# Kernel optimization log

Measured on AMD Instinct MI355X. Metric: run time of the kernel, lower is better.

The kernel has to match this reference:

```python
import jax, jax.numpy as jnp
import numpy as np

COST_CLASS, COST_MASK, COST_DICE = 2.0, 5.0, 5.0
NUM_POINTS = 12544

def setup_inputs() -> dict:
    key = jax.random.key(0)
    k1, k2, k3, k4, k5 = jax.random.split(key, 5)
    bs, Q, K = 4, 100, 134
    H = W = 256
    M = 80
    P = H * W
    pred_logits = jax.random.normal(k1, (bs, Q, K), dtype=jnp.float32)
    pred_masks = jax.random.normal(k2, (bs, Q, H, W), dtype=jnp.float32)
    tgt_labels = jax.random.randint(k3, (M,), 0, K - 1, dtype=jnp.int32)
    # binary target masks, stored as float (matches .float() in torch code)
    tgt_masks = (jax.random.uniform(k4, (M, H, W)) > 0.5).astype(jnp.float32)
    # random subset of points without replacement (torch.randperm[:num_points])
    point_idx = jax.random.permutation(k5, P)[:NUM_POINTS].astype(jnp.int32)
    return {"pred_logits": pred_logits, "pred_masks": pred_masks,
            "tgt_labels": tgt_labels, "tgt_masks": tgt_masks,
            "point_idx": point_idx}

def reference(pred_logits, pred_masks, tgt_labels, tgt_masks, point_idx):
    bs, Q, K = pred_logits.shape
    N = bs * Q
    M = tgt_masks.shape[0]
    Pn = point_idx.shape[0]

    # class cost: -p[n, tgt_id[m]]
    out_prob = jax.nn.softmax(pred_logits.reshape(N, K), axis=-1)
    tgt_ids = jnp.clip(tgt_labels.astype(jnp.int32), 0, K - 1)
    cost_class = -out_prob[:, tgt_ids]                      # (N, M)

    # sampled mask logits / targets
    x = pred_masks.reshape(N, -1)[:, point_idx]             # (N, Pn) logits
    y = tgt_masks.reshape(M, -1)[:, point_idx]              # (M, Pn) binary float

    # BCE-with-logits cost, separable form:
    # mean_p[softplus(x) - x*y] = mean_p softplus(x) - (x @ y^T)/Pn
    sp_mean = jnp.mean(jax.nn.softplus(x), axis=-1)         # (N,)
    xy = jnp.einsum('np,mp->nm', x, y)                      # (N, M)
    cost_mask = sp_mean[:, None] - xy / Pn

    # dice cost
    s = jax.nn.sigmoid(x)                                   # (N, Pn)
    numer = 2.0 * jnp.einsum('np,mp->nm', s, y)             # (N, M)
    denom = jnp.sum(s, axis=-1)[:, None] + jnp.sum(y, axis=-1)[None, :]
    cost_dice = 1.0 - (numer + 1.0) / (denom + 1.0)

    C = COST_CLASS * cost_class + COST_MASK * cost_mask + COST_DICE * cost_dice
    return C.reshape(bs, Q, M)
```

## Files before the change

kernel.cpp:

```cpp
#include <hip/hip_runtime.h>
#include <math.h>

#define N_ROWS 400
#define M_ROWS 80
#define K_CLS  134
#define PN     12544
#define PFULL  65536
#define NSUB   25
#define TSTEPS 392
#define KSPLIT 196
#define TPB    2

#define ZB_BLOCKS 33
#define GY_BLOCKS 245

typedef __attribute__((ext_vector_type(4))) float  f32x4;
typedef __attribute__((ext_vector_type(8))) __bf16 bf16x8;

__device__ __forceinline__ float wave_reduce_sum(float v) {
#pragma unroll
    for (int off = 32; off > 0; off >>= 1) v += __shfl_down(v, off, 64);
    return v;
}

__global__ __launch_bounds__(1024) void sort_softmax_kernel(
        const int* __restrict__ point_idx, int* __restrict__ sel,
        const float* __restrict__ pred_logits,
        float* __restrict__ rowmax, float* __restrict__ rowsum) {
    int tid = threadIdx.x;
    if (blockIdx.x == 0) {
        __shared__ unsigned int bits[PFULL / 32];
        __shared__ int wtot[16], wbase[16];
        bits[tid] = 0u; bits[tid + 1024] = 0u;
        __syncthreads();
        for (int i = tid; i < PN; i += 1024) {
            int p = point_idx[i];
            atomicOr(&bits[p >> 5], 1u << (p & 31));
        }
        __syncthreads();
        unsigned int w0 = bits[tid * 2], w1 = bits[tid * 2 + 1];
        int cnt = __popc(w0) + __popc(w1);
        int lane = tid & 63, wid = tid >> 6;
        int v = cnt;
#pragma unroll
        for (int off = 1; off < 64; off <<= 1) {
            int u = __shfl_up(v, off, 64);
            if (lane >= off) v += u;
        }
        if (lane == 63) wtot[wid] = v;
        __syncthreads();
        if (tid == 0) {
            int run = 0;
#pragma unroll
            for (int i = 0; i < 16; ++i) { wbase[i] = run; run += wtot[i]; }
        }
        __syncthreads();
        int base = wbase[wid] + (v - cnt);
        int p0 = tid * 64;
        while (w0) { int b = __builtin_ctz(w0); w0 &= w0 - 1; sel[base++] = p0 + b; }
        p0 += 32;
        while (w1) { int b = __builtin_ctz(w1); w1 &= w1 - 1; sel[base++] = p0 + b; }
    } else {
        int wave = tid >> 6, lane = tid & 63;
        int n = (blockIdx.x - 1) * 16 + wave;
        const float* row = pred_logits + n * K_CLS;
        float mx = -1e30f;
        for (int k = lane; k < K_CLS; k += 64) mx = fmaxf(mx, row[k]);
#pragma unroll
        for (int off = 32; off > 0; off >>= 1) mx = fmaxf(mx, __shfl_down(mx, off, 64));
        mx = __shfl(mx, 0, 64);
        float se = 0.f;
        for (int k = lane; k < K_CLS; k += 64) se += expf(row[k] - mx);
        se = wave_reduce_sum(se);
        if (lane == 0) { rowmax[n] = mx; rowsum[n] = se; }
    }
}

__global__ __launch_bounds__(512) void stage1b_kernel(
        const float* __restrict__ tgt_masks, const int* __restrict__ sel,
        __bf16* __restrict__ Yb, float* __restrict__ ypart,
        float* __restrict__ zero_region, int zero_n4) {
    __shared__ float smem[128];
    int b = blockIdx.x;
    if (b < ZB_BLOCKS) {
        int i = b * 512 + threadIdx.x;
        if (i < zero_n4) {
            f32x4 z = {0.f, 0.f, 0.f, 0.f};
            ((f32x4*)zero_region)[i] = z;
        }
        return;
    }
    int bb = b - ZB_BLOCKS;
    int j = bb / 49, tch = bb % 49;
    int wave = threadIdx.x >> 6, lane = threadIdx.x & 63;
    int colL = lane & 15, quad = lane >> 4;
    int m = 16 * j + colL;
    int t = tch * 8 + wave;
    int k0 = t * 32 + quad * 8;
    const float* yrow = tgt_masks + (size_t)m * PFULL;
    int idx[8];
    *(int4*)(idx)     = *(const int4*)(sel + k0);
    *(int4*)(idx + 4) = *(const int4*)(sel + k0 + 4);
    bf16x8 v; float acc = 0.f;
#pragma unroll
    for (int jj = 0; jj < 8; ++jj) {
        float y = yrow[idx[jj]];
        v[jj] = (__bf16)y;
        acc += y;
    }
    ((bf16x8*)Yb)[(size_t)(t * 5 + j) * 64 + lane] = v;
    acc += __shfl_down(acc, 32, 64);
    acc += __shfl_down(acc, 16, 64);
    if (quad == 0) smem[wave * 16 + colL] = acc;
    __syncthreads();
    if (threadIdx.x < 16) {
        float s = 0.f;
#pragma unroll
        for (int wv = 0; wv < 8; ++wv) s += smem[wv * 16 + threadIdx.x];
        ypart[tch * M_ROWS + 16 * j + threadIdx.x] = s;
    }
}

__global__ __launch_bounds__(256) void gemm_fused_kernel(
        const float* __restrict__ pred_masks, const int* __restrict__ sel,
        const __bf16* __restrict__ Yb,
        float* __restrict__ xyacc, float* __restrict__ syacc,
        float* __restrict__ spsum, float* __restrict__ ssum) {
    int wave = threadIdx.x >> 6, lane = threadIdx.x & 63;
    int flat = blockIdx.x * 4 + wave;
    int nsub = flat / KSPLIT, kc = flat % KSPLIT;
    int n0 = nsub * 16;
    int colL = lane & 15, quad = lane >> 4;
    int tbase = kc * TPB;

    const float* row = pred_masks + (size_t)(n0 + colL) * PFULL;
    const bf16x8* Yfrag = (const bf16x8*)Yb;

    f32x4 accX[5], accS[5];
    f32x4 zero = {0.f, 0.f, 0.f, 0.f};
#pragma unroll
    for (int j = 0; j < 5; ++j) { accX[j] = zero; accS[j] = zero; }
    float sumS = 0.f, sumSP = 0.f;

    float xs[TPB][8];
    bf16x8 Bbuf[TPB][5];
#pragma unroll
    for (int i = 0; i < TPB; ++i) {
        int t = tbase + i;
        int k0 = t * 32 + quad * 8;
        int idx[8];
        *(int4*)(idx)     = *(const int4*)(sel + k0);
        *(int4*)(idx + 4) = *(const int4*)(sel + k0 + 4);
#pragma unroll
        for (int jj = 0; jj < 8; ++jj) xs[i][jj] = row[idx[jj]];
        const bf16x8* q = Yfrag + (size_t)(t * 5) * 64 + lane;
#pragma unroll
        for (int j = 0; j < 5; ++j) Bbuf[i][j] = q[(size_t)j * 64];
    }
#pragma unroll
    for (int i = 0; i < TPB; ++i) {
        bf16x8 aX, aS;
#pragma unroll
        for (int jj = 0; jj < 8; ++jj) {
            float x  = xs[i][jj];
            float ax = fabsf(x);
            float e  = __expf(-ax);
            float inv = __builtin_amdgcn_rcpf(1.f + e);
            float sig = (x >= 0.f) ? inv : e * inv;
            float sp  = fmaxf(x, 0.f) + __logf(1.f + e);
            aX[jj] = (__bf16)x; aS[jj] = (__bf16)sig;
            sumS += sig; sumSP += sp;
        }
#pragma unroll
        for (int j = 0; j < 5; ++j) {
            accX[j] = __builtin_amdgcn_mfma_f32_16x16x32_bf16(aX, Bbuf[i][j], accX[j], 0, 0, 0);
            accS[j] = __builtin_amdgcn_mfma_f32_16x16x32_bf16(aS, Bbuf[i][j], accS[j], 0, 0, 0);
        }
    }

#pragma unroll
    for (int j = 0; j < 5; ++j)
#pragma unroll
        for (int r = 0; r < 4; ++r) {
            int n = n0 + quad * 4 + r;
            int m = 16 * j + colL;
            atomicAdd(&xyacc[n * M_ROWS + m], accX[j][r]);
            atomicAdd(&syacc[n * M_ROWS + m], accS[j][r]);
        }
    sumS  += __shfl_down(sumS, 32, 64);
    sumS  += __shfl_down(sumS, 16, 64);
    sumSP += __shfl_down(sumSP, 32, 64);
    sumSP += __shfl_down(sumSP, 16, 64);
    if (lane < 16) {
        atomicAdd(&ssum[n0 + lane], sumS);
        atomicAdd(&spsum[n0 + lane], sumSP);
    }
}

__global__ void combine_kernel(const float* __restrict__ logits,
                               const int* __restrict__ tgt_labels,
                               const float* __restrict__ rowmax,
                               const float* __restrict__ rowsum,
                               const float* __restrict__ spsum,
                               const float* __restrict__ ssum,
                               const float* __restrict__ ypart,
                               const float* __restrict__ xyacc,
                               const float* __restrict__ syacc,
                               float* __restrict__ out) {
    int idx = blockIdx.x * blockDim.x + threadIdx.x;
    if (idx >= N_ROWS * M_ROWS) return;
    int n = idx / M_ROWS, m = idx % M_ROWS;
    float ysum = 0.f;
#pragma unroll
    for (int t = 0; t < 49; ++t) ysum += ypart[t * M_ROWS + m];
    int tid = tgt_labels[m];
    tid = min(max(tid, 0), K_CLS - 1);
    float p = expf(logits[n * K_CLS + tid] - rowmax[n]) / rowsum[n];
    float cost_class = -p;
    float cost_mask = (spsum[n] - xyacc[idx]) * (1.0f / PN);
    float cost_dice = 1.f - (2.f * syacc[idx] + 1.f) / (ssum[n] + ysum + 1.f);
    out[idx] = 2.f * cost_class + 5.f * cost_mask + 5.f * cost_dice;
}

extern "C" void kernel_launch(void* const* d_in, const int* in_sizes, int n_in,
                              void* d_out, int out_size, void* d_ws, size_t ws_size,
                              hipStream_t stream) {
    const float* pred_logits = (const float*)d_in[0];
    const float* pred_masks  = (const float*)d_in[1];
    const int*   tgt_labels  = (const int*)d_in[2];
    const float* tgt_masks   = (const float*)d_in[3];
    const int*   point_idx   = (const int*)d_in[4];
    float* out = (float*)d_out;

    char* ws = (char*)d_ws;
    size_t off = 0;
    auto carve = [&](size_t nbytes) {
        char* p = ws + off;
        off += (nbytes + 255) & ~(size_t)255;
        return p;
    };
    float* xyacc = (float*)carve((size_t)N_ROWS * M_ROWS * 4);
    float* syacc = (float*)carve((size_t)N_ROWS * M_ROWS * 4);
    float* spsum = (float*)carve(N_ROWS * 4);
    float* ssum  = (float*)carve(N_ROWS * 4);
    int zero_n4 = (int)(off / 16);
    int*   sel    = (int*)carve(PN * 4);
    float* rowmax = (float*)carve(N_ROWS * 4);
    float* rowsum = (float*)carve(N_ROWS * 4);
    float* ypart  = (float*)carve(49 * M_ROWS * 4);
    __bf16* Yb = (__bf16*)carve((size_t)TSTEPS * 5 * 1024);
    (void)ws_size; (void)in_sizes; (void)n_in; (void)out_size;

    sort_softmax_kernel<<<26, 1024, 0, stream>>>(point_idx, sel, pred_logits, rowmax, rowsum);
    stage1b_kernel<<<ZB_BLOCKS + GY_BLOCKS, 512, 0, stream>>>(
        tgt_masks, sel, Yb, ypart, xyacc, zero_n4);
    gemm_fused_kernel<<<NSUB * KSPLIT / 4, 256, 0, stream>>>(
        pred_masks, sel, Yb, xyacc, syacc, spsum, ssum);
    combine_kernel<<<(N_ROWS * M_ROWS + 255) / 256, 256, 0, stream>>>(
        pred_logits, tgt_labels, rowmax, rowsum, spsum, ssum, ypart, xyacc, syacc, out);
}
```

Measured before the change: 223.8 us.

## Replace global atomics with in-block LDS reduction and per-chunk partial buffers

The GEMM kernel now reduces its four waves' MFMA accumulators and row sums through shared memory and writes deterministic per-k-group partial results instead of issuing many global float atomics. The combine kernel sums the 49 partial slices, and the zero-initialisation blocks are removed from the gather kernel. This is meant to cut atomic contention and the zeroing work. The cost is extra partial-buffer traffic (about 12.5 MB written and then read back) and an LDS buffer of roughly 40 KB per block, which may reduce occupancy.

After: 217.1 us. 1.03x faster.

```diff
diff --git a/kernel.cpp b/kernel.cpp
--- a/kernel.cpp
+++ b/kernel.cpp
@@ -10,8 +10,8 @@
 #define TSTEPS 392
 #define KSPLIT 196
 #define TPB    2
-
-#define ZB_BLOCKS 33
+#define KCG    49
+
 #define GY_BLOCKS 245
 
 typedef __attribute__((ext_vector_type(4))) float  f32x4;
@@ -76,22 +76,12 @@
     }
 }
 
-__global__ __launch_bounds__(512) void stage1b_kernel(
+__global__ __launch_bounds__(512) void gather_y_kernel(
         const float* __restrict__ tgt_masks, const int* __restrict__ sel,
-        __bf16* __restrict__ Yb, float* __restrict__ ypart,
-        float* __restrict__ zero_region, int zero_n4) {
+        __bf16* __restrict__ Yb, float* __restrict__ ypart) {
     __shared__ float smem[128];
     int b = blockIdx.x;
-    if (b < ZB_BLOCKS) {
-        int i = b * 512 + threadIdx.x;
-        if (i < zero_n4) {
-            f32x4 z = {0.f, 0.f, 0.f, 0.f};
-            ((f32x4*)zero_region)[i] = z;
-        }
-        return;
-    }
-    int bb = b - ZB_BLOCKS;
-    int j = bb / 49, tch = bb % 49;
+    int j = b / 49, tch = b % 49;
     int wave = threadIdx.x >> 6, lane = threadIdx.x & 63;
     int colL = lane & 15, quad = lane >> 4;
     int m = 16 * j + colL;
@@ -124,11 +114,13 @@
 __global__ __launch_bounds__(256) void gemm_fused_kernel(
         const float* __restrict__ pred_masks, const int* __restrict__ sel,
         const __bf16* __restrict__ Yb,
-        float* __restrict__ xyacc, float* __restrict__ syacc,
-        float* __restrict__ spsum, float* __restrict__ ssum) {
+        float* __restrict__ xypart, float* __restrict__ sypart,
+        float* __restrict__ rowS, float* __restrict__ rowSP) {
+    __shared__ float red[4][40][64];
+    __shared__ float rowred[4][2][16];
     int wave = threadIdx.x >> 6, lane = threadIdx.x & 63;
-    int flat = blockIdx.x * 4 + wave;
-    int nsub = flat / KSPLIT, kc = flat % KSPLIT;
+    int nsub = blockIdx.x / KCG, kcg = blockIdx.x % KCG;
+    int kc = kcg * 4 + wave;
     int n0 = nsub * 16;
     int colL = lane & 15, quad = lane >> 4;
     int tbase = kc * TPB;
@@ -182,18 +174,33 @@
     for (int j = 0; j < 5; ++j)
 #pragma unroll
         for (int r = 0; r < 4; ++r) {
-            int n = n0 + quad * 4 + r;
-            int m = 16 * j + colL;
-            atomicAdd(&xyacc[n * M_ROWS + m], accX[j][r]);
-            atomicAdd(&syacc[n * M_ROWS + m], accS[j][r]);
+            red[wave][j * 4 + r][lane]      = accX[j][r];
+            red[wave][20 + j * 4 + r][lane] = accS[j][r];
         }
     sumS  += __shfl_down(sumS, 32, 64);
     sumS  += __shfl_down(sumS, 16, 64);
     sumSP += __shfl_down(sumSP, 32, 64);
     sumSP += __shfl_down(sumSP, 16, 64);
-    if (lane < 16) {
-        atomicAdd(&ssum[n0 + lane], sumS);
-        atomicAdd(&spsum[n0 + lane], sumSP);
+    if (lane < 16) { rowred[wave][0][lane] = sumS; rowred[wave][1][lane] = sumSP; }
+    __syncthreads();
+#pragma unroll
+    for (int v0 = 0; v0 < 10; ++v0) {
+        int v = wave * 10 + v0;
+        float s = red[0][v][lane] + red[1][v][lane] + red[2][v][lane] + red[3][v][lane];
+        int vv = (v < 20) ? v : v - 20;
+        int j = vv >> 2, r = vv & 3;
+        int n = n0 + quad * 4 + r, m = 16 * j + colL;
+        float* dst = (v < 20) ? xypart : sypart;
+        dst[(size_t)kcg * (N_ROWS * M_ROWS) + n * M_ROWS + m] = s;
+    }
+    if (threadIdx.x < 16) {
+        rowS[kcg * N_ROWS + n0 + threadIdx.x] =
+            rowred[0][0][threadIdx.x] + rowred[1][0][threadIdx.x] +
+            rowred[2][0][threadIdx.x] + rowred[3][0][threadIdx.x];
+    } else if (threadIdx.x < 32) {
+        int l = threadIdx.x - 16;
+        rowSP[kcg * N_ROWS + n0 + l] =
+            rowred[0][1][l] + rowred[1][1][l] + rowred[2][1][l] + rowred[3][1][l];
     }
 }
 
@@ -201,24 +208,30 @@
                                const int* __restrict__ tgt_labels,
                                const float* __restrict__ rowmax,
                                const float* __restrict__ rowsum,
-                               const float* __restrict__ spsum,
-                               const float* __restrict__ ssum,
+                               const float* __restrict__ rowS,
+                               const float* __restrict__ rowSP,
                                const float* __restrict__ ypart,
-                               const float* __restrict__ xyacc,
-                               const float* __restrict__ syacc,
+                               const float* __restrict__ xypart,
+                               const float* __restrict__ sypart,
                                float* __restrict__ out) {
     int idx = blockIdx.x * blockDim.x + threadIdx.x;
     if (idx >= N_ROWS * M_ROWS) return;
     int n = idx / M_ROWS, m = idx % M_ROWS;
-    float ysum = 0.f;
-#pragma unroll
-    for (int t = 0; t < 49; ++t) ysum += ypart[t * M_ROWS + m];
+    float xy = 0.f, sy = 0.f, ssumv = 0.f, spsumv = 0.f, ysum = 0.f;
+#pragma unroll 7
+    for (int g = 0; g < KCG; ++g) {
+        xy += xypart[(size_t)g * (N_ROWS * M_ROWS) + idx];
+        sy += sypart[(size_t)g * (N_ROWS * M_ROWS) + idx];
+        ssumv  += rowS[g * N_ROWS + n];
+        spsumv += rowSP[g * N_ROWS + n];
+        ysum += ypart[g * M_ROWS + m];
+    }
     int tid = tgt_labels[m];
     tid = min(max(tid, 0), K_CLS - 1);
     float p = expf(logits[n * K_CLS + tid] - rowmax[n]) / rowsum[n];
     float cost_class = -p;
-    float cost_mask = (spsum[n] - xyacc[idx]) * (1.0f / PN);
-    float cost_dice = 1.f - (2.f * syacc[idx] + 1.f) / (ssum[n] + ysum + 1.f);
+    float cost_mask = (spsumv - xy) * (1.0f / PN);
+    float cost_dice = 1.f - (2.f * sy + 1.f) / (ssumv + ysum + 1.f);
     out[idx] = 2.f * cost_class + 5.f * cost_mask + 5.f * cost_dice;
 }
 
@@ -239,23 +252,21 @@
         off += (nbytes + 255) & ~(size_t)255;
         return p;
     };
-    float* xyacc = (float*)carve((size_t)N_ROWS * M_ROWS * 4);
-    float* syacc = (float*)carve((size_t)N_ROWS * M_ROWS * 4);
-    float* spsum = (float*)carve(N_ROWS * 4);
-    float* ssum  = (float*)carve(N_ROWS * 4);
-    int zero_n4 = (int)(off / 16);
     int*   sel    = (int*)carve(PN * 4);
     float* rowmax = (float*)carve(N_ROWS * 4);
     float* rowsum = (float*)carve(N_ROWS * 4);
-    float* ypart  = (float*)carve(49 * M_ROWS * 4);
+    float* ypart  = (float*)carve(KCG * M_ROWS * 4);
+    float* rowS   = (float*)carve(KCG * N_ROWS * 4);
+    float* rowSP  = (float*)carve(KCG * N_ROWS * 4);
+    float* xypart = (float*)carve((size_t)KCG * N_ROWS * M_ROWS * 4);
+    float* sypart = (float*)carve((size_t)KCG * N_ROWS * M_ROWS * 4);
     __bf16* Yb = (__bf16*)carve((size_t)TSTEPS * 5 * 1024);
     (void)ws_size; (void)in_sizes; (void)n_in; (void)out_size;
 
     sort_softmax_kernel<<<26, 1024, 0, stream>>>(point_idx, sel, pred_logits, rowmax, rowsum);
-    stage1b_kernel<<<ZB_BLOCKS + GY_BLOCKS, 512, 0, stream>>>(
-        tgt_masks, sel, Yb, ypart, xyacc, zero_n4);
-    gemm_fused_kernel<<<NSUB * KSPLIT / 4, 256, 0, stream>>>(
-        pred_masks, sel, Yb, xyacc, syacc, spsum, ssum);
+    gather_y_kernel<<<GY_BLOCKS, 512, 0, stream>>>(tgt_masks, sel, Yb, ypart);
+    gemm_fused_kernel<<<NSUB * KCG, 256, 0, stream>>>(
+        pred_masks, sel, Yb, xypart, sypart, rowS, rowSP);
     combine_kernel<<<(N_ROWS * M_ROWS + 255) / 256, 256, 0, stream>>>(
-        pred_logits, tgt_labels, rowmax, rowsum, spsum, ssum, ypart, xyacc, syacc, out);
-}
+        pred_logits, tgt_labels, rowmax, rowsum, rowS, rowSP, ypart, xypart, sypart, out);
+}
```
